# Kernel optimization log

Measured on AMD Instinct MI355X. Metric: run time of the kernel, lower is better.

Reference implementation:

```python
import jax, jax.numpy as jnp
import numpy as np

B, C, H, W = 1, 256, 80, 100
CB = C // 2          # bottleneck channels of NonLocalBlock
NCLS = 80            # cfg.MODEL.FCOS.NUM_CLASSES - 1


def conv1x1(x, w, b):
    # x: (B,Ci,H,W), w: (Co,Ci,1,1)
    return jnp.einsum('bihw,oi->bohw', x, w[:, :, 0, 0]) + b[None, :, None, None]


def conv3x3(x, w, b):
    y = jax.lax.conv_general_dilated(x, w, (1, 1), 'SAME',
                                     dimension_numbers=('NCHW', 'OIHW', 'NCHW'))
    return y + b[None, :, None, None]


def nonlocal_block(x, tw, tb, pw, pb, gw, gb, ww, wb):
    # Faithful to the torch code: RAW reshapes (row-major), batch is flattened
    # into the attention dimension.
    b, c, h, w = x.shape
    theta = conv1x1(x, tw, tb).reshape(-1, CB)      # (B*H*W, CB) raw order
    phi = conv1x1(x, pw, pb).reshape(CB, -1)        # (CB, B*H*W) raw order
    g = conv1x1(x, gw, gb).reshape(-1, CB)          # (B*H*W, CB)
    attn = jax.nn.softmax(theta @ phi, axis=1)      # (N, N), N = B*H*W
    y = (attn @ g).reshape(b, -1, h, w)             # (B, CB, H, W) raw order
    return conv1x1(y, ww, wb) + x


def kp_head(x, w1, b1, w2, b2):
    # Convolution(3, C, C, with_bn=False): conv3x3 + bias + ReLU, then 1x1 conv
    return conv1x1(jax.nn.relu(conv3x3(x, w1, b1)), w2, b2)


def setup_inputs() -> dict:
    key = jax.random.key(0)
    ks = iter(jax.random.split(key, 64))
    def nrm(shape, std=0.01):
        return jax.random.normal(next(ks), shape, dtype=jnp.float32) * std
    inp = {'feature': jax.random.normal(next(ks), (B, C, H, W), dtype=jnp.float32)}
    for p in ('tlnl', 'brnl'):
        inp[p + '_tw'] = nrm((CB, C, 1, 1)); inp[p + '_tb'] = jnp.zeros((CB,), jnp.float32)
        inp[p + '_pw'] = nrm((CB, C, 1, 1)); inp[p + '_pb'] = jnp.zeros((CB,), jnp.float32)
        inp[p + '_gw'] = nrm((CB, C, 1, 1)); inp[p + '_gb'] = jnp.zeros((CB,), jnp.float32)
        inp[p + '_ww'] = nrm((C, CB, 1, 1)); inp[p + '_wb'] = jnp.zeros((C,), jnp.float32)
    for name, od in (('tl_heat', NCLS), ('br_heat', NCLS), ('tl_tag', 1),
                     ('br_tag', 1), ('tl_regr', 2), ('br_regr', 2)):
        inp[name + '_w1'] = nrm((C, C, 3, 3)); inp[name + '_b1'] = jnp.zeros((C,), jnp.float32)
        inp[name + '_w2'] = nrm((od, C, 1, 1))
        bias = -2.19 if 'heat' in name else 0.0   # heat bias init in torch code
        inp[name + '_b2'] = jnp.full((od,), bias, jnp.float32)
    return inp


def reference(feature,
              tlnl_tw, tlnl_tb, tlnl_pw, tlnl_pb, tlnl_gw, tlnl_gb, tlnl_ww, tlnl_wb,
              brnl_tw, brnl_tb, brnl_pw, brnl_pb, brnl_gw, brnl_gb, brnl_ww, brnl_wb,
              tl_heat_w1, tl_heat_b1, tl_heat_w2, tl_heat_b2,
              br_heat_w1, br_heat_b1, br_heat_w2, br_heat_b2,
              tl_tag_w1, tl_tag_b1, tl_tag_w2, tl_tag_b2,
              br_tag_w1, br_tag_b1, br_tag_w2, br_tag_b2,
              tl_regr_w1, tl_regr_b1, tl_regr_w2, tl_regr_b2,
              br_regr_w1, br_regr_b1, br_regr_w2, br_regr_b2):
    tl_nl = nonlocal_block(feature, tlnl_tw, tlnl_tb, tlnl_pw, tlnl_pb,
                           tlnl_gw, tlnl_gb, tlnl_ww, tlnl_wb)
    br_nl = nonlocal_block(feature, brnl_tw, brnl_tb, brnl_pw, brnl_pb,
                           brnl_gw, brnl_gb, brnl_ww, brnl_wb)
    tl_heat = kp_head(tl_nl, tl_heat_w1, tl_heat_b1, tl_heat_w2, tl_heat_b2)
    br_heat = kp_head(br_nl, br_heat_w1, br_heat_b1, br_heat_w2, br_heat_b2)
    tl_tag = kp_head(tl_nl, tl_tag_w1, tl_tag_b1, tl_tag_w2, tl_tag_b2)
    br_tag = kp_head(br_nl, br_tag_w1, br_tag_b1, br_tag_w2, br_tag_b2)
    tl_regr = kp_head(tl_nl, tl_regr_w1, tl_regr_b1, tl_regr_w2, tl_regr_b2)
    br_regr = kp_head(br_nl, br_regr_w1, br_regr_b1, br_regr_w2, br_regr_b2)
    return (tl_heat, br_heat, tl_tag, br_tag, tl_regr, br_regr)
```

## Files before the change

### kernel.cpp

```cpp
#include <hip/hip_runtime.h>
#include <hip/hip_bf16.h>
#include <math.h>
#include <type_traits>

#define NPIX 8000
#define IMH 80
#define IMW 100
#define PW 104
#define PH 82

typedef __attribute__((ext_vector_type(8))) short short8v;
typedef __attribute__((ext_vector_type(4))) short short4v;
typedef __attribute__((ext_vector_type(4))) float f32x4;
typedef __attribute__((ext_vector_type(4))) unsigned int u32x4;

__device__ inline short f2bf(float f) {
    __hip_bfloat16 h = __float2bfloat16(f);
    return *reinterpret_cast<short*>(&h);
}
__device__ inline float bf2f(short s) {
    __hip_bfloat16 h;
    *reinterpret_cast<short*>(&h) = s;
    return __bfloat162float(h);
}
__device__ inline unsigned int cvt_pk_bf16(float lo, float hi) {
    unsigned int d;
    asm volatile("v_cvt_pk_bf16_f32 %0, %1, %2" : "=v"(d) : "v"(lo), "v"(hi));
    return d;
}

__global__ __launch_bounds__(256) void zero_k(float4* __restrict__ p, int n)
{
    int i = blockIdx.x * 256 + threadIdx.x;
    int stride = gridDim.x * 256;
    float4 z = {0.f, 0.f, 0.f, 0.f};
    for (; i < n; i += stride) p[i] = z;
}

__global__ __launch_bounds__(256) void featT_k(
    const float* __restrict__ feat, short* __restrict__ featT)
{
    __shared__ float ts[64][65];
    const int tid = threadIdx.x;
    const int p0 = blockIdx.x * 64, c0 = blockIdx.y * 64;
#pragma unroll
    for (int it = 0; it < 16; it++) {
        int f = it * 256 + tid;
        int ci = f >> 6, px = f & 63;
        ts[px][ci] = feat[(size_t)(c0 + ci) * NPIX + p0 + px];
    }
    __syncthreads();
#pragma unroll
    for (int it = 0; it < 2; it++) {
        int f = it * 256 + tid;
        int px = f >> 3, c8 = f & 7;
        short8v v;
#pragma unroll
        for (int j = 0; j < 8; j++) v[j] = f2bf(ts[px][c8 * 8 + j]);
        *(short8v*)(featT + (size_t)(p0 + px) * 256 + c0 + c8 * 8) = v;
    }
}

struct W8 { const float* s[8]; short* d[8]; };
__global__ __launch_bounds__(256) void prep_w8_k(W8 a)
{
    const int z = blockIdx.y;
    const float* s = a.s[z];
    short* d = a.d[z];
    int i = (blockIdx.x * 256 + threadIdx.x) * 4;
    if (i < 32768) {
        float4 v = *(const float4*)(s + i);
        short4v o;
        o[0] = f2bf(v.x); o[1] = f2bf(v.y); o[2] = f2bf(v.z); o[3] = f2bf(v.w);
        *(short4v*)(d + i) = o;
    }
}

__global__ __launch_bounds__(256) void wt2_k(
    const float* __restrict__ w0, const float* __restrict__ w1,
    const float* __restrict__ w2, const float* __restrict__ w3,
    const float* __restrict__ w4, const float* __restrict__ w5,
    short* __restrict__ Wt)
{
    const int h = blockIdx.y;
    const float* w = (h == 0) ? w0 : (h == 1) ? w1 : (h == 2) ? w2
                   : (h == 3) ? w3 : (h == 4) ? w4 : w5;
    const int co = blockIdx.x;
    const int tid = threadIdx.x;
    __shared__ float lt[2304];
    for (int e = tid; e < 2304; e += 256)
        lt[e] = w[(size_t)co * 2304 + e];
    __syncthreads();
    short* dst = Wt + ((size_t)(h * 256 + co) * 9) * 256;
#pragma unroll
    for (int tap = 0; tap < 9; tap++)
        dst[tap * 256 + tid] = f2bf(lt[tid * 9 + tap]);
}

__global__ __launch_bounds__(256) void qkv_mfma_k(
    const short* __restrict__ featT, const short* __restrict__ wqkv,
    const float* __restrict__ bq0, const float* __restrict__ bq1,
    const float* __restrict__ bq2, const float* __restrict__ bq3,
    const float* __restrict__ bq4, const float* __restrict__ bq5,
    short* __restrict__ th0, short* __restrict__ ph0, short* __restrict__ g0,
    short* __restrict__ th1, short* __restrict__ ph1, short* __restrict__ g1)
{
    __shared__ __align__(16) short As[64 * 40];
    __shared__ __align__(16) short Bs[160 * 40];

    const int tid = threadIdx.x;
    const int bx = blockIdx.x;
    const int co0 = (bx / 50) * 64;
    const int p0 = (bx % 50) * 160;
    const int w = tid >> 6, l = tid & 63, lg = l >> 4, li = l & 15;

    f32x4 acc[4][3] = {};

    for (int cb = 0; cb < 8; cb++) {
        __syncthreads();
        {
            int co = tid >> 2, c8 = tid & 3;
            *(short8v*)(As + co * 40 + c8 * 8) =
                *(const short8v*)(wqkv + (size_t)(co0 + co) * 256 + cb * 32 + c8 * 8);
        }
        for (int e = tid; e < 640; e += 256) {
            int px = e >> 2, c8 = e & 3;
            *(short8v*)(Bs + px * 40 + c8 * 8) =
                *(const short8v*)(featT + (size_t)(p0 + px) * 256 + cb * 32 + c8 * 8);
        }
        __syncthreads();

        short8v af[4];
#pragma unroll
        for (int m = 0; m < 4; m++)
            af[m] = *(const short8v*)(As + (m * 16 + li) * 40 + lg * 8);
#pragma unroll
        for (int t = 0; t < 3; t++) {
            int n = w + 4 * t;
            if (n < 10) {
                short8v bf = *(const short8v*)(Bs + (n * 16 + li) * 40 + lg * 8);
#pragma unroll
                for (int m = 0; m < 4; m++)
                    acc[m][t] = __builtin_amdgcn_mfma_f32_16x16x32_bf16(
                        af[m], bf, acc[m][t], 0, 0, 0);
            }
        }
    }

    const int idx6 = co0 >> 7;
    const int sub = co0 & 127;
    const int kind = idx6 % 3;
    const float* bias = (idx6 == 0) ? bq0 : (idx6 == 1) ? bq1 : (idx6 == 2) ? bq2
                      : (idx6 == 3) ? bq3 : (idx6 == 4) ? bq4 : bq5;
    short* cm = (idx6 == 0) ? th0 : (idx6 == 2) ? g0
              : (idx6 == 3) ? th1 : g1;
    short* ph = (idx6 == 1) ? ph0 : ph1;

#pragma unroll
    for (int m = 0; m < 4; m++) {
#pragma unroll
        for (int t = 0; t < 3; t++) {
            int n = w + 4 * t;
            if (n < 10) {
                int p = p0 + n * 16 + li;
#pragma unroll
                for (int j = 0; j < 4; j++) {
                    int co = sub + m * 16 + lg * 4 + j;
                    float v = acc[m][t][j] + bias[co];
                    if (kind == 1)
                        ph[(size_t)p * 128 + co] = f2bf(v);
                    else
                        cm[(size_t)co * NPIX + p] = f2bf(v);
                }
            }
        }
    }
}

__global__ __launch_bounds__(256) void transp_k(
    const short* __restrict__ g0, short* __restrict__ o0,
    const short* __restrict__ g1, short* __restrict__ o1)
{
    const short* G = blockIdx.z ? g1 : g0;
    short* O = blockIdx.z ? o1 : o0;
    __shared__ __align__(16) short ts[64][68];
    const int tid = threadIdx.x;
    const int q0 = blockIdx.x * 64, d0 = blockIdx.y * 64;

#pragma unroll
    for (int k = 0; k < 4; k++) {
        int f = k * 256 + tid;
        int q = f >> 4, d4 = f & 15;
        *(short4v*)&ts[q][d4 * 4] =
            *(const short4v*)(G + (size_t)(q0 + q) * 128 + d0 + d4 * 4);
    }
    __syncthreads();
#pragma unroll
    for (int k = 0; k < 4; k++) {
        int f = k * 256 + tid;
        int d = f >> 4, q4 = f & 15;
        short4v v;
        v[0] = ts[q4 * 4 + 0][d];
        v[1] = ts[q4 * 4 + 1][d];
        v[2] = ts[q4 * 4 + 2][d];
        v[3] = ts[q4 * 4 + 3][d];
        *(short4v*)(O + (size_t)(d0 + d) * NPIX + q0 + q4 * 4) = v;
    }
}

__global__ __launch_bounds__(256) void flash2_k(
    const short* __restrict__ th0, const short* __restrict__ pT0,
    const short* __restrict__ gT0,
    const short* __restrict__ th1, const short* __restrict__ pT1,
    const short* __restrict__ gT1,
    short* __restrict__ ohb, float* __restrict__ mlb)
{
    const int id = blockIdx.x;
    const int xcd = id & 7;
    const int combo = xcd >> 1;
    const int pb = combo >> 1, half = combo & 1;
    const int qi = ((id >> 3) << 1) + (xcd & 1);
    if (qi * 128 >= NPIX) return;

    const short* TH = pb ? th1 : th0;
    const short* PT = pb ? pT1 : pT0;
    const short* GT = pb ? gT1 : gT0;
    short* OH = ohb + (size_t)(pb * 2 + half) * 1024000;
    float* ML = mlb + (size_t)(pb * 2 + half) * 16000;
    const int t0 = half ? 63 : 0;
    const int t1 = half ? 125 : 63;

    const int tid = threadIdx.x;
    const int w = tid >> 6, l = tid & 63, lg = l >> 4, li = l & 15;
    const int qb0 = qi * 128 + w * 32;

    short8v qf[2][4];
#pragma unroll
    for (int nq = 0; nq < 2; nq++)
#pragma unroll
        for (int ks = 0; ks < 4; ks++)
            qf[nq][ks] = *(const short8v*)(TH + (size_t)(qb0 + nq * 16 + li) * 128
                                            + ks * 32 + lg * 8);

    f32x4 acc_ot[8][2] = {};
    float mj[2] = {-1e30f, -1e30f};
    float lj[2] = {0.f, 0.f};

    for (int t = t0; t < t1; ++t) {
        const int kv0 = t * 64;

        f32x4 s[4][2] = {};
#pragma unroll
        for (int mk = 0; mk < 4; mk++) {
            short8v kf[4];
#pragma unroll
            for (int ks = 0; ks < 4; ks++)
                kf[ks] = *(const short8v*)(PT + (size_t)(kv0 + mk * 16 + li) * 128
                                            + ks * 32 + lg * 8);
#pragma unroll
            for (int ks = 0; ks < 4; ks++)
#pragma unroll
                for (int nq = 0; nq < 2; nq++)
                    s[mk][nq] = __builtin_amdgcn_mfma_f32_16x16x32_bf16(
                        kf[ks], qf[nq][ks], s[mk][nq], 0, 0, 0);
        }

        unsigned int pk[4][2][2];
#pragma unroll
        for (int nq = 0; nq < 2; nq++) {
            float sm = -1e30f;
#pragma unroll
            for (int mk = 0; mk < 4; mk++)
#pragma unroll
                for (int j = 0; j < 4; j++) sm = fmaxf(sm, s[mk][nq][j]);
            sm = fmaxf(sm, __shfl_xor(sm, 16));
            sm = fmaxf(sm, __shfl_xor(sm, 32));
            float mo = mj[nq];
            float mn = fmaxf(mo, sm);
            float sc = __expf(mo - mn);
            mj[nq] = mn;
            float ps = 0.f;
#pragma unroll
            for (int mk = 0; mk < 4; mk++) {
#pragma unroll
                for (int j = 0; j < 4; j++) {
                    float pe = __expf(s[mk][nq][j] - mn);
                    s[mk][nq][j] = pe;
                    ps += pe;
                }
                pk[mk][nq][0] = cvt_pk_bf16(s[mk][nq][0], s[mk][nq][1]);
                pk[mk][nq][1] = cvt_pk_bf16(s[mk][nq][2], s[mk][nq][3]);
            }
            ps += __shfl_xor(ps, 16);
            ps += __shfl_xor(ps, 32);
            lj[nq] = lj[nq] * sc + ps;
#pragma unroll
            for (int md = 0; md < 8; md++) acc_ot[md][nq] *= sc;
        }

#pragma unroll
        for (int ks = 0; ks < 2; ks++) {
            short8v vf[8];
#pragma unroll
            for (int md = 0; md < 8; md++)
                vf[md] = *(const short8v*)(GT + (size_t)(md * 16 + li) * NPIX
                                            + kv0 + ks * 32 + lg * 8);
            short8v br[2];
#pragma unroll
            for (int nq = 0; nq < 2; nq++) {
                u32x4 bw;
#pragma unroll
                for (int wi = 0; wi < 4; wi++) {
                    int lgs = ((lg & 1) << 1) + (wi >> 1);
                    int src = li + (lgs << 4);
                    unsigned int a0 = (unsigned int)__shfl(
                        (int)pk[2 * ks][nq][wi & 1], src, 64);
                    unsigned int a1 = (unsigned int)__shfl(
                        (int)pk[2 * ks + 1][nq][wi & 1], src, 64);
                    bw[wi] = (lg >> 1) ? a1 : a0;
                }
                br[nq] = __builtin_bit_cast(short8v, bw);
            }
#pragma unroll
            for (int md = 0; md < 8; md++)
#pragma unroll
                for (int nq = 0; nq < 2; nq++)
                    acc_ot[md][nq] = __builtin_amdgcn_mfma_f32_16x16x32_bf16(
                        vf[md], br[nq], acc_ot[md][nq], 0, 0, 0);
        }
    }

#pragma unroll
    for (int nq = 0; nq < 2; nq++) {
        int q = qb0 + nq * 16 + li;
        if (q < NPIX) {
            float linv = 1.f / lj[nq];
#pragma unroll
            for (int md = 0; md < 8; md++) {
                short4v o4;
#pragma unroll
                for (int jj = 0; jj < 4; jj++)
                    o4[jj] = f2bf(acc_ot[md][nq][jj] * linv);
                *(short4v*)(OH + (size_t)q * 128 + md * 16 + lg * 4) = o4;
            }
            if (lg == 0) {
                ML[q] = mj[nq];
                ML[8000 + q] = lj[nq];
            }
        }
    }
}

__global__ __launch_bounds__(256, 2) void flash5_k(
    const short* __restrict__ th0, const short* __restrict__ pT0,
    const short* __restrict__ gT0,
    const short* __restrict__ th1, const short* __restrict__ pT1,
    const short* __restrict__ gT1,
    short* __restrict__ ohb, float* __restrict__ mlb)
{
    __shared__ __align__(16) short Ks[64 * 128];
    __shared__ __align__(16) short Vs[128 * 64];

    const int id = blockIdx.x;
    const int combo = id & 7;
    const int pb = combo >> 2, part = combo & 3;
    const int qi = id >> 3;

    const short* TH = pb ? th1 : th0;
    const short* PT = pb ? pT1 : pT0;
    const short* GT = pb ? gT1 : gT0;
    short* OH = ohb + (size_t)(pb * 4 + part) * 1024000;
    float* ML = mlb + (size_t)(pb * 4 + part) * 16000;
    const int t0 = (part == 0) ? 0 : (part == 1) ? 32 : (part == 2) ? 63 : 94;
    const int t1 = (part == 0) ? 32 : (part == 1) ? 63 : (part == 2) ? 94 : 125;

    const int tid = threadIdx.x;
    const int w = tid >> 6, l = tid & 63, lg = l >> 4, li = l & 15;
    const int qb0 = qi * 128 + w * 32;

    short8v qf[2][4];
#pragma unroll
    for (int nq = 0; nq < 2; nq++)
#pragma unroll
        for (int ks = 0; ks < 4; ks++)
            qf[nq][ks] = *(const short8v*)(TH + (size_t)(qb0 + nq * 16 + li) * 128
                                            + ks * 32 + lg * 8);

    f32x4 acc_ot[8][2] = {};
    float lj[2] = {0.f, 0.f};

    const int swz = (li & 7) << 3;

    for (int t = t0; t < t1; ++t) {
        const int kv0 = t * 64;

        __syncthreads();
#pragma unroll
        for (int i = 0; i < 4; i++) {
            int ch = i * 256 + tid;
            int row = ch >> 4, c = ch & 15;
            *(short8v*)(Ks + row * 128 + ((c * 8) ^ ((row & 7) << 3))) =
                *(const short8v*)(PT + (size_t)(kv0 + row) * 128 + c * 8);
        }
#pragma unroll
        for (int i = 0; i < 4; i++) {
            int ch = i * 256 + tid;
            int row = ch >> 3, c = ch & 7;
            *(short8v*)(Vs + row * 64 + ((c * 8) ^ ((row & 7) << 3))) =
                *(const short8v*)(GT + (size_t)row * NPIX + kv0 + c * 8);
        }
        __syncthreads();

        unsigned int pk[4][2][2];
#pragma unroll
        for (int mk = 0; mk < 4; mk++) {
            short8v kf[4];
#pragma unroll
            for (int ks = 0; ks < 4; ks++)
                kf[ks] = *(const short8v*)(Ks + (mk * 16 + li) * 128
                                            + ((ks * 32 + lg * 8) ^ swz));
            f32x4 s[2] = {};
#pragma unroll
            for (int ks = 0; ks < 4; ks++)
#pragma unroll
                for (int nq = 0; nq < 2; nq++)
                    s[nq] = __builtin_amdgcn_mfma_f32_16x16x32_bf16(
                        kf[ks], qf[nq][ks], s[nq], 0, 0, 0);
#pragma unroll
            for (int nq = 0; nq < 2; nq++) {
                float e0 = __expf(s[nq][0]);
                float e1 = __expf(s[nq][1]);
                float e2 = __expf(s[nq][2]);
                float e3 = __expf(s[nq][3]);
                lj[nq] += (e0 + e1) + (e2 + e3);
                pk[mk][nq][0] = cvt_pk_bf16(e0, e1);
                pk[mk][nq][1] = cvt_pk_bf16(e2, e3);
            }
        }

#pragma unroll
        for (int ks = 0; ks < 2; ks++) {
            short8v br[2];
#pragma unroll
            for (int nq = 0; nq < 2; nq++) {
                u32x4 bw;
#pragma unroll
                for (int wi = 0; wi < 4; wi++) {
                    int lgs = ((lg & 1) << 1) + (wi >> 1);
                    int src = li + (lgs << 4);
                    unsigned int a0 = (unsigned int)__shfl(
                        (int)pk[2 * ks][nq][wi & 1], src, 64);
                    unsigned int a1 = (unsigned int)__shfl(
                        (int)pk[2 * ks + 1][nq][wi & 1], src, 64);
                    bw[wi] = (lg >> 1) ? a1 : a0;
                }
                br[nq] = __builtin_bit_cast(short8v, bw);
            }
#pragma unroll
            for (int md = 0; md < 8; md++) {
                short8v vf = *(const short8v*)(Vs + (md * 16 + li) * 64
                                                + ((ks * 32 + lg * 8) ^ swz));
#pragma unroll
                for (int nq = 0; nq < 2; nq++)
                    acc_ot[md][nq] = __builtin_amdgcn_mfma_f32_16x16x32_bf16(
                        vf, br[nq], acc_ot[md][nq], 0, 0, 0);
            }
        }
    }

#pragma unroll
    for (int nq = 0; nq < 2; nq++) {
        lj[nq] += __shfl_xor(lj[nq], 16);
        lj[nq] += __shfl_xor(lj[nq], 32);
    }
#pragma unroll
    for (int nq = 0; nq < 2; nq++) {
        int q = qb0 + nq * 16 + li;
        if (q < NPIX) {
            float linv = 1.f / lj[nq];
#pragma unroll
            for (int md = 0; md < 8; md++) {
                short4v o4;
#pragma unroll
                for (int jj = 0; jj < 4; jj++)
                    o4[jj] = f2bf(acc_ot[md][nq][jj] * linv);
                *(short4v*)(OH + (size_t)q * 128 + md * 16 + lg * 4) = o4;
            }
            if (lg == 0) {
                ML[q] = 0.f;
                ML[8000 + q] = lj[nq];
            }
        }
    }
}

__global__ __launch_bounds__(256) void combine_k(
    const short* __restrict__ ohb, const float* __restrict__ mlb,
    short* __restrict__ ybb)
{
    const int tid = threadIdx.x;
    const int r0 = blockIdx.x * 64;
    const int prob = blockIdx.y;
    const short* o0 = ohb + (size_t)(prob * 2) * 1024000;
    const short* o1 = o0 + 1024000;
    const float* ml0 = mlb + (size_t)(prob * 2) * 16000;
    const float* ml1 = ml0 + 16000;
    short* yb = ybb + (size_t)prob * 1024000;

#pragma unroll
    for (int it = 0; it < 4; it++) {
        int e = it * 256 + tid;
        int r = r0 + (e >> 4), c8 = e & 15;
        float m0 = ml0[r], l0 = ml0[8000 + r];
        float m1 = ml1[r], l1 = ml1[8000 + r];
        float mm = fmaxf(m0, m1);
        float a0 = l0 * __expf(m0 - mm);
        float a1 = l1 * __expf(m1 - mm);
        float inv = 1.f / (a0 + a1);
        short8v v0 = *(const short8v*)(o0 + (size_t)r * 128 + c8 * 8);
        short8v v1 = *(const short8v*)(o1 + (size_t)r * 128 + c8 * 8);
        short8v o;
#pragma unroll
        for (int j = 0; j < 8; j++)
            o[j] = f2bf((a0 * bf2f(v0[j]) + a1 * bf2f(v1[j])) * inv);
        *(short8v*)(yb + (size_t)r * 128 + c8 * 8) = o;
    }
}

__global__ __launch_bounds__(256) void combine4_k(
    const short* __restrict__ ohb, const float* __restrict__ mlb,
    short* __restrict__ ybb)
{
    const int tid = threadIdx.x;
    const int r0 = blockIdx.x * 64;
    const int prob = blockIdx.y;
    const short* O[4];
    const float* ML[4];
#pragma unroll
    for (int i = 0; i < 4; i++) {
        O[i] = ohb + (size_t)(prob * 4 + i) * 1024000;
        ML[i] = mlb + (size_t)(prob * 4 + i) * 16000;
    }
    short* yb = ybb + (size_t)prob * 1024000;

#pragma unroll
    for (int it = 0; it < 4; it++) {
        int e = it * 256 + tid;
        int r = r0 + (e >> 4), c8 = e & 15;
        float mm = -1e30f;
#pragma unroll
        for (int i = 0; i < 4; i++) mm = fmaxf(mm, ML[i][r]);
        float a[4], ssum = 0.f;
#pragma unroll
        for (int i = 0; i < 4; i++) {
            a[i] = ML[i][8000 + r] * __expf(ML[i][r] - mm);
            ssum += a[i];
        }
        float inv = 1.f / ssum;
        float acc[8] = {};
#pragma unroll
        for (int i = 0; i < 4; i++) {
            short8v v = *(const short8v*)(O[i] + (size_t)r * 128 + c8 * 8);
#pragma unroll
            for (int j = 0; j < 8; j++) acc[j] += a[i] * bf2f(v[j]);
        }
        short8v o;
#pragma unroll
        for (int j = 0; j < 8; j++) o[j] = f2bf(acc[j] * inv);
        *(short8v*)(yb + (size_t)r * 128 + c8 * 8) = o;
    }
}

__global__ __launch_bounds__(256) void wconv_mfma_k(
    const short* __restrict__ yb0, const short* __restrict__ yb1,
    const short* __restrict__ wcv,
    const float* __restrict__ bw0, const float* __restrict__ bw1,
    const short* __restrict__ featT,
    short* __restrict__ nlp0, short* __restrict__ nlp1)
{
    __shared__ __align__(16) short Ys[64 * 136];
    __shared__ __align__(16) short Ws[64 * 136];

    const int tid = threadIdx.x;
    const int prob = blockIdx.z;
    const short* yb = prob ? yb1 : yb0;
    const short* wc = wcv + (size_t)prob * 32768;
    const float* bw = prob ? bw1 : bw0;
    short* nlp = prob ? nlp1 : nlp0;

    const int p0 = blockIdx.x * 64;
    const int co0 = blockIdx.y * 64;
    const int w = tid >> 6, l = tid & 63, lg = l >> 4, li = l & 15;

#pragma unroll
    for (int it = 0; it < 4; it++) {
        int f = it * 256 + tid;
        int px = f >> 4, c8 = f & 15;
        *(short8v*)(Ys + px * 136 + c8 * 8) =
            *(const short8v*)(yb + (size_t)(p0 + px) * 128 + c8 * 8);
    }
#pragma unroll
    for (int it = 0; it < 4; it++) {
        int f = it * 256 + tid;
        int co = f >> 4, c8 = f & 15;
        *(short8v*)(Ws + co * 136 + c8 * 8) =
            *(const short8v*)(wc + (size_t)(co0 + co) * 128 + c8 * 8);
    }
    __syncthreads();

    f32x4 acc[4] = {};
#pragma unroll
    for (int ks = 0; ks < 4; ks++) {
        short8v af = *(const short8v*)(Ys + (w * 16 + li) * 136 + ks * 32 + lg * 8);
#pragma unroll
        for (int n = 0; n < 4; n++) {
            short8v bf = *(const short8v*)(Ws + (n * 16 + li) * 136 + ks * 32 + lg * 8);
            acc[n] = __builtin_amdgcn_mfma_f32_16x16x32_bf16(af, bf, acc[n], 0, 0, 0);
        }
    }

#pragma unroll
    for (int n = 0; n < 4; n++) {
#pragma unroll
        for (int j = 0; j < 4; j++) {
            int p = p0 + w * 16 + lg * 4 + j;
            int co = co0 + n * 16 + li;
            float v = acc[n][j] + bw[co] + bf2f(featT[(size_t)p * 256 + co]);
            int y = p / 100;
            int x = p - y * 100;
            size_t ppx = (size_t)(y + 1) * PW + (x + 1);
            nlp[ppx * 256 + co] = f2bf(v);
        }
    }
}

struct H6 {
    const short* rb[6];
    const float* w[6];
    const float* b[6];
    float* o[6];
    int co[6];
};

__global__ __launch_bounds__(256) void head_mfma6_k(H6 a, int hbase)
{
    const int k = hbase + blockIdx.z;
    const short* x = a.rb[k];
    const float* w = a.w[k];
    const float* b = a.b[k];
    float* out     = a.o[k];
    const int Co   = a.co[k];

    const int tid = threadIdx.x;
    const int wv = tid >> 6, l = tid & 63, lg = l >> 4, li = l & 15;
    const int p0 = blockIdx.x * 64 + wv * 16;

    short8v bf[8];
#pragma unroll
    for (int ks = 0; ks < 8; ks++)
        bf[ks] = *(const short8v*)(x + (size_t)(p0 + li) * 256 + ks * 32 + lg * 8);

    const int nmt = (Co + 15) >> 4;
    for (int mt = 0; mt < nmt; mt++) {
        const int row = mt * 16 + li;
        f32x4 acc = {};
#pragma unroll
        for (int ks = 0; ks < 8; ks++) {
            short8v af;
            if (row < Co) {
                const float* wp = w + (size_t)row * 256 + ks * 32 + lg * 8;
                float4 a0 = *(const float4*)wp;
                float4 a1 = *(const float4*)(wp + 4);
                af[0] = f2bf(a0.x); af[1] = f2bf(a0.y);
                af[2] = f2bf(a0.z); af[3] = f2bf(a0.w);
                af[4] = f2bf(a1.x); af[5] = f2bf(a1.y);
                af[6] = f2bf(a1.z); af[7] = f2bf(a1.w);
            } else {
                af = short8v{0, 0, 0, 0, 0, 0, 0, 0};
            }
            acc = __builtin_amdgcn_mfma_f32_16x16x32_bf16(af, bf[ks], acc, 0, 0, 0);
        }
#pragma unroll
        for (int j = 0; j < 4; j++) {
            int co = mt * 16 + lg * 4 + j;
            if (co < Co)
                out[(size_t)co * NPIX + p0 + li] = acc[j] + b[co];
        }
    }
}

#define ASTR 296
#define BSTR 1680

struct C6 { const float* bias[6]; short* rb[6]; };

__global__ __launch_bounds__(512) void conv3x3_mfma6_k(
    const short* __restrict__ nl0, const short* __restrict__ nl1,
    const short* __restrict__ Wt, C6 c, int hbase)
{
    __shared__ __align__(16) short As[64 * ASTR];
    __shared__ __align__(16) short Bs[10 * BSTR];

    const int tid = threadIdx.x;
    const int h = hbase + blockIdx.y;
    const short* nlp = (h & 1) ? nl1 : nl0;
    const float* bs = c.bias[h];
    const short* wth = Wt + (size_t)h * 256 * 9 * 256;
    short* out = c.rb[h];

    const int bx = blockIdx.x;
    const int co0 = (bx / 20) * 64;
    const int rem = bx % 20;
    const int y0 = (rem >> 1) * 8;
    const int x0 = (rem & 1) * 50;

    const int w = tid >> 6, l = tid & 63, lg = l >> 4, li = l & 15;
    const int rr = li >> 1, cc = li & 1;

    f32x4 acc[4][4] = {};

    const int bbase = (rr + 1) * BSTR + (cc + 1) * 32 + lg * 8;
    const int abase = li * ASTR + lg * 8;

    for (int cb = 0; cb < 8; cb++) {
        __syncthreads();
        for (int e = tid; e < 2080; e += 512) {
            int c8 = e & 3;
            int pos = e >> 2;
            int row = pos / 52;
            int col = pos - row * 52;
            *(short8v*)(Bs + row * BSTR + col * 32 + c8 * 8) =
                *(const short8v*)(nlp + ((size_t)(y0 + row) * PW + x0 + col) * 256
                                  + cb * 32 + c8 * 8);
        }
        for (int e = tid; e < 2304; e += 512) {
            int c8 = e & 3;
            int pos = e >> 2;
            int co = pos / 9;
            int tap = pos - co * 9;
            *(short8v*)(As + co * ASTR + tap * 32 + c8 * 8) =
                *(const short8v*)(wth + ((size_t)(co0 + co) * 9 + tap) * 256
                                  + cb * 32 + c8 * 8);
        }
        __syncthreads();

#pragma unroll
        for (int tap = 0; tap < 9; tap++) {
            const int dy = tap / 3 - 1, dx = tap % 3 - 1;
            short8v af[4];
#pragma unroll
            for (int m = 0; m < 4; m++)
                af[m] = *(const short8v*)(As + abase + m * 16 * ASTR + tap * 32);
            const int boff = bbase + dy * BSTR + dx * 32;
#pragma unroll
            for (int t = 0; t < 4; t++) {
                int n = w + 8 * t;
                if (n < 25) {
                    short8v bf = *(const short8v*)(Bs + boff + n * 64);
#pragma unroll
                    for (int m = 0; m < 4; m++)
                        acc[m][t] = __builtin_amdgcn_mfma_f32_16x16x32_bf16(
                            af[m], bf, acc[m][t], 0, 0, 0);
                }
            }
        }
    }

#pragma unroll
    for (int m = 0; m < 4; m++) {
#pragma unroll
        for (int t = 0; t < 4; t++) {
            int n = w + 8 * t;
            if (n < 25) {
                int xo = x0 + n * 2 + cc;
                int yo = y0 + rr;
                int px = yo * IMW + xo;
                int cob = co0 + m * 16 + lg * 4;
                short4v o4;
#pragma unroll
                for (int j = 0; j < 4; j++)
                    o4[j] = f2bf(fmaxf(acc[m][t][j] + bs[cob + j], 0.f));
                *(short4v*)(out + (size_t)px * 256 + cob) = o4;
            }
        }
    }
}

extern "C" void kernel_launch(void* const* d_in, const int* in_sizes, int n_in,
                              void* d_out, int out_size, void* d_ws, size_t ws_size,
                              hipStream_t stream)
{
    const float* feat = (const float*)d_in[0];
    auto F = [&](int i) { return (const float*)d_in[i]; };

    float* out = (float*)d_out;
    char* base = (char*)d_ws;

    short* featT  = (short*)(base);
    short* wcv    = (short*)(base + 4096000);
    short* wqkv   = (short*)(base + 4227072);
    short* thb[2] = {(short*)(base + 4620288),  (short*)(base + 10813440)};
    short* phT[2] = {(short*)(base + 6717440),  (short*)(base + 12910592)};
    short* gb[2]  = {(short*)(base + 8765440),  (short*)(base + 14958592)};
    short* gT[2]  = {(short*)(base + 17006592), (short*)(base + 19054592)};
    short* ohb    = (short*)(base + 21102592);
    float* mlb    = (float*)(base + 29294592);
    short* ohb4   = (short*)(base + 29550592);
    float* mlb4   = (float*)(base + 45934592);
    const bool split4 = ws_size >= (size_t)46446592;
    short* yb[2]  = {(short*)(base + 4620288), (short*)(base + 6668288)};
    short* Wt     = (short*)(base + 8716288);
    short* nlp0   = (short*)(base + 15794176);
    short* nlp1   = (short*)(base + 20160512);
    short* rbp[6];
    rbp[0] = (short*)(base + 0);
    rbp[1] = (short*)(base + 4096000);
    rbp[2] = (short*)(base + 24526848);
    rbp[3] = (short*)(base + 29550592);
    rbp[4] = (short*)(base + 33646592);
    rbp[5] = (short*)(base + 37742592);

    featT_k<<<dim3(125, 4), 256, 0, stream>>>(feat, featT);

    W8 wa;
    wa.s[0] = F(1);  wa.s[1] = F(3);  wa.s[2] = F(5);
    wa.s[3] = F(9);  wa.s[4] = F(11); wa.s[5] = F(13);
    wa.s[6] = F(7);  wa.s[7] = F(15);
    for (int z = 0; z < 6; z++) wa.d[z] = wqkv + (size_t)z * 32768;
    wa.d[6] = wcv; wa.d[7] = wcv + 32768;
    prep_w8_k<<<dim3(32, 8), 256, 0, stream>>>(wa);

    zero_k<<<12, 256, 0, stream>>>((float4*)((char*)thb[0] + 2048000), 3072);
    zero_k<<<12, 256, 0, stream>>>((float4*)((char*)thb[1] + 2048000), 3072);

    qkv_mfma_k<<<dim3(600), 256, 0, stream>>>(
        featT, wqkv, F(2), F(4), F(6), F(10), F(12), F(14),
        thb[0], phT[0], gb[0], thb[1], phT[1], gb[1]);

    transp_k<<<dim3(125, 2, 2), 256, 0, stream>>>(gb[0], gT[0], gb[1], gT[1]);

    if (split4) {
        flash5_k<<<dim3(504), 256, 0, stream>>>(
            thb[0], phT[0], gT[0], thb[1], phT[1], gT[1], ohb4, mlb4);
        combine4_k<<<dim3(125, 2), 256, 0, stream>>>(ohb4, mlb4, yb[0]);
    } else {
        flash2_k<<<dim3(256), 256, 0, stream>>>(
            thb[0], phT[0], gT[0], thb[1], phT[1], gT[1], ohb, mlb);
        combine_k<<<dim3(125, 2), 256, 0, stream>>>(ohb, mlb, yb[0]);
    }

    wt2_k<<<dim3(256, 6), 256, 0, stream>>>(
        F(17), F(21), F(25), F(29), F(33), F(37), Wt);

    zero_k<<<1024, 256, 0, stream>>>((float4*)nlp0, 545792);
    wconv_mfma_k<<<dim3(125, 4, 2), 256, 0, stream>>>(
        yb[0], yb[1], wcv, F(8), F(16), featT, nlp0, nlp1);

    struct HD { size_t off; int co; };
    const HD hd[6] = { {0u, 80}, {640000u, 80}, {1280000u, 1},
                       {1288000u, 1}, {1296000u, 2}, {1312000u, 2} };

    C6 c;
    H6 a;
    for (int h = 0; h < 6; h++) {
        c.bias[h] = F(18 + 4 * h);
        a.w[h] = F(19 + 4 * h);
        a.b[h] = F(20 + 4 * h);
        a.o[h] = out + hd[h].off;
        a.co[h] = hd[h].co;
    }

    if (split4) {
        for (int h = 0; h < 6; h++) { c.rb[h] = rbp[h]; a.rb[h] = rbp[h]; }
        conv3x3_mfma6_k<<<dim3(80, 6), 512, 0, stream>>>(nlp0, nlp1, Wt, c, 0);
        head_mfma6_k<<<dim3(125, 1, 6), 256, 0, stream>>>(a, 0);
    } else {
        for (int h = 0; h < 6; h++) { c.rb[h] = rbp[h % 3]; a.rb[h] = rbp[h % 3]; }
        conv3x3_mfma6_k<<<dim3(80, 3), 512, 0, stream>>>(nlp0, nlp1, Wt, c, 0);
        head_mfma6_k<<<dim3(125, 1, 3), 256, 0, stream>>>(a, 0);
        conv3x3_mfma6_k<<<dim3(80, 3), 512, 0, stream>>>(nlp0, nlp1, Wt, c, 3);
        head_mfma6_k<<<dim3(125, 1, 3), 256, 0, stream>>>(a, 3);
    }
}
```

Before: 231.8 us.

## Double-buffer K/V tiles in split flash kernel with register prefetch

Converts the split-4 flash attention kernel to double-buffered LDS for the K and V tiles. The next tile's global loads are issued into registers before the current tile's MFMA work and written to the alternate buffer afterwards, so only one barrier per iteration remains. This aims to hide global memory latency behind compute. In exchange it doubles LDS use to 64KB per block and adds 32 VGPRs of prefetch registers, which may limit occupancy at launch_bounds(256,2).

```diff
diff --git a/kernel.cpp b/kernel.cpp
--- a/kernel.cpp
+++ b/kernel.cpp
@@ -351,15 +351,15 @@
     }
 }
 
-__global__ __launch_bounds__(256, 2) void flash5_k(
+__global__ __launch_bounds__(256, 2) void flash6_k(
     const short* __restrict__ th0, const short* __restrict__ pT0,
     const short* __restrict__ gT0,
     const short* __restrict__ th1, const short* __restrict__ pT1,
     const short* __restrict__ gT1,
     short* __restrict__ ohb, float* __restrict__ mlb)
 {
-    __shared__ __align__(16) short Ks[64 * 128];
-    __shared__ __align__(16) short Vs[128 * 64];
+    __shared__ __align__(16) short Ks[2][64 * 128];
+    __shared__ __align__(16) short Vs[2][128 * 64];
 
     const int id = blockIdx.x;
     const int combo = id & 7;
@@ -378,6 +378,16 @@
     const int w = tid >> 6, l = tid & 63, lg = l >> 4, li = l & 15;
     const int qb0 = qi * 128 + w * 32;
 
+    int krow[4], kc[4], vrow[4], vc[4], kdst[4], vdst[4];
+#pragma unroll
+    for (int i = 0; i < 4; i++) {
+        int ch = i * 256 + tid;
+        krow[i] = ch >> 4; kc[i] = ch & 15;
+        kdst[i] = krow[i] * 128 + ((kc[i] * 8) ^ ((krow[i] & 7) << 3));
+        vrow[i] = ch >> 3; vc[i] = ch & 7;
+        vdst[i] = vrow[i] * 64 + ((vc[i] * 8) ^ ((vrow[i] & 7) << 3));
+    }
+
     short8v qf[2][4];
 #pragma unroll
     for (int nq = 0; nq < 2; nq++)
@@ -391,25 +401,34 @@
 
     const int swz = (li & 7) << 3;
 
+    {
+        const int kv0 = t0 * 64;
+#pragma unroll
+        for (int i = 0; i < 4; i++)
+            *(short8v*)(Ks[0] + kdst[i]) =
+                *(const short8v*)(PT + (size_t)(kv0 + krow[i]) * 128 + kc[i] * 8);
+#pragma unroll
+        for (int i = 0; i < 4; i++)
+            *(short8v*)(Vs[0] + vdst[i]) =
+                *(const short8v*)(GT + (size_t)vrow[i] * NPIX + kv0 + vc[i] * 8);
+    }
+    __syncthreads();
+
     for (int t = t0; t < t1; ++t) {
-        const int kv0 = t * 64;
-
-        __syncthreads();
-#pragma unroll
-        for (int i = 0; i < 4; i++) {
-            int ch = i * 256 + tid;
-            int row = ch >> 4, c = ch & 15;
-            *(short8v*)(Ks + row * 128 + ((c * 8) ^ ((row & 7) << 3))) =
-                *(const short8v*)(PT + (size_t)(kv0 + row) * 128 + c * 8);
-        }
-#pragma unroll
-        for (int i = 0; i < 4; i++) {
-            int ch = i * 256 + tid;
-            int row = ch >> 3, c = ch & 7;
-            *(short8v*)(Vs + row * 64 + ((c * 8) ^ ((row & 7) << 3))) =
-                *(const short8v*)(GT + (size_t)row * NPIX + kv0 + c * 8);
-        }
-        __syncthreads();
+        const int cur = (t - t0) & 1;
+        const int nxt = cur ^ 1;
+        const bool pf = (t + 1) < t1;
+
+        short8v kpf[4], vpf[4];
+        if (pf) {
+            const int kn = (t + 1) * 64;
+#pragma unroll
+            for (int i = 0; i < 4; i++)
+                kpf[i] = *(const short8v*)(PT + (size_t)(kn + krow[i]) * 128 + kc[i] * 8);
+#pragma unroll
+            for (int i = 0; i < 4; i++)
+                vpf[i] = *(const short8v*)(GT + (size_t)vrow[i] * NPIX + kn + vc[i] * 8);
+        }
 
         unsigned int pk[4][2][2];
 #pragma unroll
@@ -417,7 +436,7 @@
             short8v kf[4];
 #pragma unroll
             for (int ks = 0; ks < 4; ks++)
-                kf[ks] = *(const short8v*)(Ks + (mk * 16 + li) * 128
+                kf[ks] = *(const short8v*)(Ks[cur] + (mk * 16 + li) * 128
                                             + ((ks * 32 + lg * 8) ^ swz));
             f32x4 s[2] = {};
 #pragma unroll
@@ -458,7 +477,7 @@
             }
 #pragma unroll
             for (int md = 0; md < 8; md++) {
-                short8v vf = *(const short8v*)(Vs + (md * 16 + li) * 64
+                short8v vf = *(const short8v*)(Vs[cur] + (md * 16 + li) * 64
                                                 + ((ks * 32 + lg * 8) ^ swz));
 #pragma unroll
                 for (int nq = 0; nq < 2; nq++)
@@ -466,6 +485,16 @@
                         vf, br[nq], acc_ot[md][nq], 0, 0, 0);
             }
         }
+
+        if (pf) {
+#pragma unroll
+            for (int i = 0; i < 4; i++)
+                *(short8v*)(Ks[nxt] + kdst[i]) = kpf[i];
+#pragma unroll
+            for (int i = 0; i < 4; i++)
+                *(short8v*)(Vs[nxt] + vdst[i]) = vpf[i];
+        }
+        __syncthreads();
     }
 
 #pragma unroll
@@ -840,7 +869,7 @@
     transp_k<<<dim3(125, 2, 2), 256, 0, stream>>>(gb[0], gT[0], gb[1], gT[1]);
 
     if (split4) {
-        flash5_k<<<dim3(504), 256, 0, stream>>>(
+        flash6_k<<<dim3(504), 256, 0, stream>>>(
             thb[0], phT[0], gT[0], thb[1], phT[1], gT[1], ohb4, mlb4);
         combine4_k<<<dim3(125, 2), 256, 0, stream>>>(ohb4, mlb4, yb[0]);
     } else {
```

New measurement: 233.9 us. No clear change (+0.9%).
